# Kernel tuning notes

Hardware: AMD Instinct MI355X
Metric: run time of the kernel (lower is better)

The kernel has to match this reference:

```python
import jax, jax.numpy as jnp
import numpy as np

B = 65536
OBS_DIM = 85          # input_shape
FEAT = 8              # dim_entity_feature
NL = 5                # dim_landmarks
NT = 10               # dim_total
INF = 64              # in_features == out_features
HID = 64              # rnn_hidden_dim
NACT = 5              # n_actions
ALPHA = 0.01


def _leaky(x):
    return jnp.where(x > 0, x, ALPHA * x)


def setup_inputs() -> dict:
    key = jax.random.key(0)
    ks = jax.random.split(key, 26)
    s = 0.1
    d = {
        'obs': jax.random.normal(ks[0], (B, OBS_DIM), jnp.float32),
        'hidden_state': jax.random.normal(ks[1], (B, HID), jnp.float32),
        # entity input projections (input_layer_0/1/2), stored [in, out]
        'w_in0': jax.random.normal(ks[2], (FEAT, INF), jnp.float32) * s,
        'b_in0': jax.random.normal(ks[3], (INF,), jnp.float32) * s,
        'w_in1': jax.random.normal(ks[4], (FEAT, INF), jnp.float32) * s,
        'b_in1': jax.random.normal(ks[5], (INF,), jnp.float32) * s,
        'w_in2': jax.random.normal(ks[6], (FEAT, INF), jnp.float32) * s,
        'b_in2': jax.random.normal(ks[7], (INF,), jnp.float32) * s,
        # GAT params
        'W': jax.random.normal(ks[8], (INF, INF), jnp.float32) * s,
        'a': jax.random.normal(ks[9], (2 * INF, 1), jnp.float32) * s,
        # output MLP on attention rows (dim_soft = 2*dim_nearby = 10)
        'w_o1': jax.random.normal(ks[10], (2 * NL, 32), jnp.float32) * s,
        'b_o1': jax.random.normal(ks[11], (32,), jnp.float32) * s,
        'w_o2': jax.random.normal(ks[12], (32, 16), jnp.float32) * s,
        'b_o2': jax.random.normal(ks[13], (16,), jnp.float32) * s,
        'w_o3': jax.random.normal(ks[14], (16, 1), jnp.float32) * s,
        'b_o3': jax.random.normal(ks[15], (1,), jnp.float32) * s,
        # fc1 takes obs (85) concat atom_plug (5) -> 90
        'w_fc1': jax.random.normal(ks[16], (OBS_DIM + NL, HID), jnp.float32) * s,
        'b_fc1': jax.random.normal(ks[17], (HID,), jnp.float32) * s,
        # GRUCell, torch layout: [3H, in]
        'w_ih': jax.random.normal(ks[18], (3 * HID, HID), jnp.float32) * s,
        'w_hh': jax.random.normal(ks[19], (3 * HID, HID), jnp.float32) * s,
        'b_ih': jax.random.normal(ks[20], (3 * HID,), jnp.float32) * s,
        'b_hh': jax.random.normal(ks[21], (3 * HID,), jnp.float32) * s,
        'w_fc2': jax.random.normal(ks[22], (HID, NACT), jnp.float32) * s,
        'b_fc2': jax.random.normal(ks[23], (NACT,), jnp.float32) * s,
    }
    return d


def reference(obs, hidden_state, w_in0, b_in0, w_in1, b_in1, w_in2, b_in2,
              W, a, w_o1, b_o1, w_o2, b_o2, w_o3, b_o3,
              w_fc1, b_fc1, w_ih, w_hh, b_ih, b_hh, w_fc2, b_fc2):
    # data_preprocess: drop last dim_nearby cols, rotate first 4 to back, reshape to entities
    o = obs[:, :OBS_DIM - NL]                               # [B, 80]
    obs_in = jnp.concatenate([o[:, 4:], o[:, :4]], axis=-1).reshape(-1, NT, FEAT)  # [B,10,8]

    h0 = _leaky(obs_in @ w_in0 + b_in0)                     # [B,10,64]
    h1 = _leaky(obs_in @ w_in1 + b_in1)
    h2 = _leaky(obs_in @ w_in2 + b_in2)
    h_mix = jnp.concatenate([h0[:, :NL], h1[:, NL:NT - 1], h2[:, NT - 1:NT]], axis=1)  # [B,10,64]

    Wh = h_mix @ W                                          # [B,10,64]
    Wh1 = Wh @ a[:INF]                                      # [B,10,1]
    Wh2 = Wh @ a[INF:]                                      # [B,10,1]
    e = _leaky(Wh1 + jnp.swapaxes(Wh2, 1, 2))               # [B,10,10]

    att0 = jax.nn.softmax(e[:, :NL, NL:], axis=-1)          # [B,5,5]
    att1 = jnp.swapaxes(jax.nn.softmax(e[:, NL:, :NL], axis=-1), 1, 2)  # [B,5,5]
    attention = jnp.concatenate([att0, att1], axis=-1)      # [B,5,10]

    hp = _leaky(attention @ w_o1 + b_o1)
    hp = _leaky(hp @ w_o2 + b_o2)
    hp = _leaky(hp @ w_o3 + b_o3)[..., 0]                   # [B,5]
    obs_out = jax.nn.softmax(hp, axis=-1)                   # [B,5]

    obs_comb = jnp.concatenate([obs, obs_out], axis=-1)     # [B,90]
    x = jax.nn.relu(obs_comb @ w_fc1 + b_fc1)               # [B,64]

    h_in = hidden_state.reshape(-1, HID)
    gi = x @ w_ih.T + b_ih                                  # [B,192]
    gh = h_in @ w_hh.T + b_hh
    r = jax.nn.sigmoid(gi[:, :HID] + gh[:, :HID])
    z = jax.nn.sigmoid(gi[:, HID:2 * HID] + gh[:, HID:2 * HID])
    n = jnp.tanh(gi[:, 2 * HID:] + r * gh[:, 2 * HID:])
    h = (1.0 - z) * n + z * h_in                            # [B,64]

    q = h @ w_fc2 + b_fc2                                   # [B,5]
    return (q, h)
```

## Files before the change

### kernel.cpp

```cpp
#include <hip/hip_runtime.h>
#include <math.h>

namespace {

typedef __bf16 bf16x8 __attribute__((ext_vector_type(8)));
typedef __bf16 bf16x4 __attribute__((ext_vector_type(4)));
typedef float  f32x4  __attribute__((ext_vector_type(4)));
typedef float  f32x2  __attribute__((ext_vector_type(2)));

constexpr int B_      = 65536;
constexpr int OBS_DIM_= 85;
constexpr int NL_     = 5;
constexpr int NT_     = 10;
constexpr int HID_    = 64;
constexpr int NACT_   = 5;
constexpr float ALPHA_= 0.01f;

__device__ __forceinline__ float leaky(float x)    { return fmaf(fminf(x, 0.0f), ALPHA_ - 1.0f, x); }
__device__ __forceinline__ float sigmoidf(float x) { return 1.0f / (1.0f + __expf(-x)); }
__device__ __forceinline__ float tanh_fast(float x){ return 1.0f - 2.0f / (__expf(2.0f * x) + 1.0f); }

template <int CTRL>
__device__ __forceinline__ float dppadd(float x) {
  int y = __builtin_amdgcn_update_dpp(0, __float_as_int(x), CTRL, 0xF, 0xF, true);
  return x + __int_as_float(y);
}
__device__ __forceinline__ float red16(float x) {
  x = dppadd<0xB1>(x);
  x = dppadd<0x4E>(x);
  x = dppadd<0x141>(x);
  x = dppadd<0x140>(x);
  return x;
}

__global__ void prep_kernel(const float* __restrict__ W, const float* __restrict__ a,
                            const float* __restrict__ w_ih, const float* __restrict__ w_hh,
                            const float* __restrict__ w_fc1, void* __restrict__ ws) {
  float* Wa   = (float*)ws;
  __bf16* ih  = (__bf16*)((char*)ws + 512);
  __bf16* hh  = ih + 192 * 64;
  __bf16* f1t = hh + 192 * 64;
  const int tid = blockIdx.x * 256 + threadIdx.x;
  if (blockIdx.x == 0 && threadIdx.x < 64) {
    const int i = threadIdx.x;
    float s1 = 0.0f, s2 = 0.0f;
    #pragma unroll
    for (int j = 0; j < 64; ++j) {
      float w = W[i * 64 + j];
      s1 += w * a[j];
      s2 += w * a[64 + j];
    }
    Wa[i] = s1;
    Wa[64 + i] = s2;
  }
  const int stride = gridDim.x * 256;
  for (int i = tid; i < 192 * 64; i += stride) {
    int pr = i >> 6, k = i & 63;
    int g  = pr >> 6;
    int q  = pr & 63;
    int orig = (g << 6) + ((q & 15) << 2) + (q >> 4);
    ih[i] = (__bf16)w_ih[orig * 64 + k];
    hh[i] = (__bf16)w_hh[orig * 64 + k];
  }
  for (int i = tid; i < 64 * 96; i += stride) {
    int n = i / 96, k = i - 96 * n;
    float v = 0.0f;
    if (k < 85)                 v = w_fc1[k * 64 + n];
    else if (k >= 88 && k < 93) v = w_fc1[(85 + k - 88) * 64 + n];
    f1t[i] = (__bf16)v;
  }
}

constexpr int SXH_ = 72;

__global__ __launch_bounds__(256, 2) void fused_kernel(
    const float* __restrict__ obs, const float* __restrict__ hidden,
    const float* __restrict__ w_in0, const float* __restrict__ b_in0,
    const float* __restrict__ w_in1, const float* __restrict__ b_in1,
    const float* __restrict__ w_in2, const float* __restrict__ b_in2,
    const float* __restrict__ w_o1, const float* __restrict__ b_o1,
    const float* __restrict__ w_o2, const float* __restrict__ b_o2,
    const float* __restrict__ w_o3, const float* __restrict__ b_o3,
    const float* __restrict__ b_fc1,
    const float* __restrict__ b_ih, const float* __restrict__ b_hh,
    const float* __restrict__ w_fc2, const float* __restrict__ b_fc2,
    const void* __restrict__ wsv,
    float* __restrict__ q_out, float* __restrict__ h_out) {

  __shared__ __align__(16) char smem[28416];
  __bf16* s_obs          = (__bf16*)smem;
  float  (*s_att)[5][10] = (float (*)[5][10])(smem + 11264);
  __bf16 (*s_h1)[5][32]  = (__bf16 (*)[5][32])(smem + 14464);
  float  (*s_h2)[5][16]  = (float (*)[5][16])(smem + 19584);
  __bf16* A_x            = (__bf16*)(smem + 11264);
  float (*s_wh1)[12]     = (float (*)[12])(smem + 24704);
  float (*s_wh2)[12]     = (float (*)[12])(smem + 25472);
  float (*s_colm)[6]     = (float (*)[6])(smem + 26240);
  float (*s_cols)[6]     = (float (*)[6])(smem + 26624);
  float (*s_hp)[6]       = (float (*)[6])(smem + 27008);
  __bf16* s_o5           = (__bf16*)(smem + 27392);

  const int tid  = threadIdx.x;
  const int wv   = tid >> 6;
  const int lane = tid & 63;
  const int l16  = lane & 15;
  const int grp  = tid >> 4;
  const long gr0 = (long)blockIdx.x * 64;

  const float* Wa = (const float*)wsv;
  const __bf16* Wih = (const __bf16*)((const char*)wsv + 512);
  const __bf16* Whh = Wih + 192 * 64;
  const __bf16* Wf1 = Whh + 192 * 64;

  {
    const float* src = obs + gr0 * OBS_DIM_;
    const int base = wv * 340;
    #pragma unroll
    for (int k = 0; k < 6; ++k) {
      if (k < 5 || lane < 20) {
        int c = base + k * 64 + lane;
        f32x4 v = *(const f32x4*)&src[c * 4];
        #pragma unroll
        for (int e = 0; e < 4; ++e) {
          int fe = c * 4 + e;
          int r = fe / 85, col = fe - 85 * r;
          s_obs[r * 88 + col] = (__bf16)v[e];
        }
      }
    }
    if (lane < 48) {
      int r = wv * 16 + lane / 3, j = lane % 3;
      s_obs[r * 88 + 85 + j] = (__bf16)0.0f;
      s_o5[r * 8 + 5 + j]    = (__bf16)0.0f;
    }
  }

  const int u0 = l16 * 4;
  const f32x4 wa1 = *(const f32x4*)&Wa[u0];
  const f32x4 wa2 = *(const f32x4*)&Wa[64 + u0];

  __syncthreads();

  #pragma unroll 1
  for (int pass = 0; pass < 4; ++pass) {
    const int row = pass * 16 + grp;
    const __bf16* orow = s_obs + row * 88;

    f32x4 wA[8];
    f32x4 bA;
    #pragma unroll
    for (int t = 0; t < NT_; ++t) {
      if (t == 0) {
        #pragma unroll
        for (int f = 0; f < 8; ++f) wA[f] = *(const f32x4*)&w_in0[f * 64 + u0];
        bA = *(const f32x4*)&b_in0[u0];
      }
      if (t == 5) {
        #pragma unroll
        for (int f = 0; f < 8; ++f) wA[f] = *(const f32x4*)&w_in1[f * 64 + u0];
        bA = *(const f32x4*)&b_in1[u0];
      }
      if (t == 9) {
        #pragma unroll
        for (int f = 0; f < 8; ++f) wA[f] = *(const f32x4*)&w_in2[f * 64 + u0];
        bA = *(const f32x4*)&b_in2[u0];
      }
      const int ia = t * 8 + 4;
      int ib = t * 8 + 8;
      if (ib >= 80) ib = 0;
      bf16x4 va = *(const bf16x4*)&orow[ia];
      bf16x4 vb = *(const bf16x4*)&orow[ib];
      float oa[4], ob[4];
      #pragma unroll
      for (int e = 0; e < 4; ++e) { oa[e] = (float)va[e]; ob[e] = (float)vb[e]; }
      f32x4 z = bA;
      #pragma unroll
      for (int f = 0; f < 4; ++f) {
        z[0] += oa[f] * wA[f][0]; z[1] += oa[f] * wA[f][1];
        z[2] += oa[f] * wA[f][2]; z[3] += oa[f] * wA[f][3];
      }
      #pragma unroll
      for (int f = 4; f < 8; ++f) {
        z[0] += ob[f - 4] * wA[f][0]; z[1] += ob[f - 4] * wA[f][1];
        z[2] += ob[f - 4] * wA[f][2]; z[3] += ob[f - 4] * wA[f][3];
      }
      float h0 = leaky(z[0]), h1 = leaky(z[1]), h2 = leaky(z[2]), h3 = leaky(z[3]);
      float p1t = h0 * wa1[0] + h1 * wa1[1] + h2 * wa1[2] + h3 * wa1[3];
      float p2t = h0 * wa2[0] + h1 * wa2[1] + h2 * wa2[2] + h3 * wa2[3];
      p1t = red16(p1t);
      p2t = red16(p2t);
      if (l16 == 0) { s_wh1[grp][t] = p1t; s_wh2[grp][t] = p2t; }
    }

    if (l16 >= 5 && l16 < 10) {
      const int jj = l16 - 5;
      float w1v = s_wh1[grp][NL_ + jj];
      float ev[NL_], m = -1e30f;
      #pragma unroll
      for (int k = 0; k < NL_; ++k) { ev[k] = leaky(w1v + s_wh2[grp][k]); m = fmaxf(m, ev[k]); }
      float s = 0.0f;
      #pragma unroll
      for (int k = 0; k < NL_; ++k) s += __expf(ev[k] - m);
      s_colm[grp][jj] = m;
      s_cols[grp][jj] = s;
    }

    if (l16 < NL_) {
      const int r = l16;
      const float wh1_r = s_wh1[grp][r];
      const float wh2_r = s_wh2[grp][r];
      float ev[NL_], m = -1e30f;
      #pragma unroll
      for (int j = 0; j < NL_; ++j) { ev[j] = leaky(wh1_r + s_wh2[grp][NL_ + j]); m = fmaxf(m, ev[j]); }
      float a0[NL_], s = 0.0f;
      #pragma unroll
      for (int j = 0; j < NL_; ++j) { a0[j] = __expf(ev[j] - m); s += a0[j]; }
      float inv = 1.0f / s;
      #pragma unroll
      for (int j = 0; j < NL_; ++j) s_att[grp][r][j] = a0[j] * inv;
      #pragma unroll
      for (int jj = 0; jj < NL_; ++jj) {
        float e = leaky(s_wh1[grp][NL_ + jj] + wh2_r);
        s_att[grp][r][NL_ + jj] = __expf(e - s_colm[grp][jj]) / s_cols[grp][jj];
      }
    }

    {
      f32x2 w1c[NT_];
      #pragma unroll
      for (int k = 0; k < NT_; ++k) w1c[k] = *(const f32x2*)&w_o1[k * 32 + l16 * 2];
      const f32x2 b1 = *(const f32x2*)&b_o1[l16 * 2];
      #pragma unroll
      for (int r5 = 0; r5 < NL_; ++r5) {
        float za = b1[0], zb = b1[1];
        #pragma unroll
        for (int k2 = 0; k2 < 5; ++k2) {
          f32x2 at = *(const f32x2*)&s_att[grp][r5][k2 * 2];
          za += at[0] * w1c[2 * k2][0] + at[1] * w1c[2 * k2 + 1][0];
          zb += at[0] * w1c[2 * k2][1] + at[1] * w1c[2 * k2 + 1][1];
        }
        s_h1[grp][r5][l16 * 2]     = (__bf16)leaky(za);
        s_h1[grp][r5][l16 * 2 + 1] = (__bf16)leaky(zb);
      }
    }

    {
      float w2c[32];
      #pragma unroll
      for (int k = 0; k < 32; ++k) w2c[k] = w_o2[k * 16 + l16];
      const float b2 = b_o2[l16];
      #pragma unroll
      for (int r5 = 0; r5 < NL_; ++r5) {
        float z = b2;
        #pragma unroll
        for (int k4 = 0; k4 < 8; ++k4) {
          bf16x4 hv = *(const bf16x4*)&s_h1[grp][r5][k4 * 4];
          z += (float)hv[0] * w2c[4 * k4] + (float)hv[1] * w2c[4 * k4 + 1]
             + (float)hv[2] * w2c[4 * k4 + 2] + (float)hv[3] * w2c[4 * k4 + 3];
        }
        s_h2[grp][r5][l16] = leaky(z);
      }
    }

    if (l16 < NL_) {
      float z3 = b_o3[0];
      #pragma unroll
      for (int k4 = 0; k4 < 4; ++k4) {
        f32x4 hv = *(const f32x4*)&s_h2[grp][l16][k4 * 4];
        z3 += hv[0] * w_o3[4 * k4] + hv[1] * w_o3[4 * k4 + 1]
            + hv[2] * w_o3[4 * k4 + 2] + hv[3] * w_o3[4 * k4 + 3];
      }
      float hp_own = leaky(z3);
      s_hp[grp][l16] = hp_own;
      float m5 = -1e30f;
      #pragma unroll
      for (int j = 0; j < NL_; ++j) m5 = fmaxf(m5, s_hp[grp][j]);
      float ssum = 0.0f;
      #pragma unroll
      for (int j = 0; j < NL_; ++j) ssum += __expf(s_hp[grp][j] - m5);
      s_o5[row * 8 + l16] = (__bf16)(__expf(hp_own - m5) / ssum);
    }
  }

  __syncthreads();

  const int l    = l16;
  const int quad = lane >> 4;
  const int r0   = wv * 16;

  bf16x8 ah[2];
  {
    const float* hrow_g = hidden + (gr0 + r0 + l) * HID_;
    f32x4 vha0 = *(const f32x4*)&hrow_g[quad * 8];
    f32x4 vha1 = *(const f32x4*)&hrow_g[quad * 8 + 4];
    f32x4 vhb0 = *(const f32x4*)&hrow_g[32 + quad * 8];
    f32x4 vhb1 = *(const f32x4*)&hrow_g[32 + quad * 8 + 4];
    bf16x8 t;
    t[0] = (__bf16)vha0[0]; t[1] = (__bf16)vha0[1]; t[2] = (__bf16)vha0[2]; t[3] = (__bf16)vha0[3];
    t[4] = (__bf16)vha1[0]; t[5] = (__bf16)vha1[1]; t[6] = (__bf16)vha1[2]; t[7] = (__bf16)vha1[3];
    ah[0] = t;
    t[0] = (__bf16)vhb0[0]; t[1] = (__bf16)vhb0[1]; t[2] = (__bf16)vhb0[2]; t[3] = (__bf16)vhb0[3];
    t[4] = (__bf16)vhb1[0]; t[5] = (__bf16)vhb1[1]; t[6] = (__bf16)vhb1[2]; t[7] = (__bf16)vhb1[3];
    ah[1] = t;
  }

  const f32x4 zero4 = {0.0f, 0.0f, 0.0f, 0.0f};

  f32x4 cx[4];
  #pragma unroll
  for (int nt = 0; nt < 4; ++nt) cx[nt] = zero4;
  #pragma unroll
  for (int ks = 0; ks < 3; ++ks) {
    bf16x8 af;
    if (ks < 2)         af = *(const bf16x8*)&s_obs[(r0 + l) * 88 + ks * 32 + quad * 8];
    else if (quad < 3)  af = *(const bf16x8*)&s_obs[(r0 + l) * 88 + 64 + quad * 8];
    else                af = *(const bf16x8*)&s_o5[(r0 + l) * 8];
    #pragma unroll
    for (int nt = 0; nt < 4; ++nt) {
      bf16x8 bf = *(const bf16x8*)&Wf1[(nt * 16 + l) * 96 + ks * 32 + quad * 8];
      cx[nt] = __builtin_amdgcn_mfma_f32_16x16x32_bf16(af, bf, cx[nt], 0, 0, 0);
    }
  }
  #pragma unroll
  for (int nt = 0; nt < 4; ++nt) {
    float bias = b_fc1[nt * 16 + l];
    #pragma unroll
    for (int rg = 0; rg < 4; ++rg) {
      float xv = fmaxf(cx[nt][rg] + bias, 0.0f);
      A_x[(r0 + quad * 4 + rg) * SXH_ + nt * 16 + l] = (__bf16)xv;
    }
  }

  bf16x8 ax[2];
  #pragma unroll
  for (int ks = 0; ks < 2; ++ks)
    ax[ks] = *(const bf16x8*)&A_x[(r0 + l) * SXH_ + ks * 32 + quad * 8];

  f32x4 cr[4], ch[4];
  #pragma unroll
  for (int nt = 0; nt < 4; ++nt) { cr[nt] = zero4; ch[nt] = zero4; }
  #pragma unroll
  for (int nt = 0; nt < 4; ++nt) {
    #pragma unroll
    for (int ks = 0; ks < 2; ++ks) {
      bf16x8 bi = *(const bf16x8*)&Wih[(nt * 16 + l) * 64 + ks * 32 + quad * 8];
      cr[nt] = __builtin_amdgcn_mfma_f32_16x16x32_bf16(ax[ks], bi, cr[nt], 0, 0, 0);
      bf16x8 bh = *(const bf16x8*)&Whh[(nt * 16 + l) * 64 + ks * 32 + quad * 8];
      cr[nt] = __builtin_amdgcn_mfma_f32_16x16x32_bf16(ah[ks], bh, cr[nt], 0, 0, 0);
    }
    #pragma unroll
    for (int ks = 0; ks < 2; ++ks) {
      bf16x8 bh = *(const bf16x8*)&Whh[(128 + nt * 16 + l) * 64 + ks * 32 + quad * 8];
      ch[nt] = __builtin_amdgcn_mfma_f32_16x16x32_bf16(ah[ks], bh, ch[nt], 0, 0, 0);
    }
  }
  f32x4 rn[4];
  {
    f32x4 a0 = *(const f32x4*)&b_ih[4 * l];
    f32x4 a1 = *(const f32x4*)&b_hh[4 * l];
    f32x4 br4 = a0 + a1;
    f32x4 bhn4 = *(const f32x4*)&b_hh[128 + 4 * l];
    #pragma unroll
    for (int nt = 0; nt < 4; ++nt)
      #pragma unroll
      for (int rg = 0; rg < 4; ++rg) {
        float rr = sigmoidf(cr[nt][rg] + br4[nt]);
        rn[nt][rg] = rr * (ch[nt][rg] + bhn4[nt]);
      }
  }

  f32x4 cn[4];
  #pragma unroll
  for (int nt = 0; nt < 4; ++nt) cn[nt] = zero4;
  #pragma unroll
  for (int nt = 0; nt < 4; ++nt)
    #pragma unroll
    for (int ks = 0; ks < 2; ++ks) {
      bf16x8 bi = *(const bf16x8*)&Wih[(128 + nt * 16 + l) * 64 + ks * 32 + quad * 8];
      cn[nt] = __builtin_amdgcn_mfma_f32_16x16x32_bf16(ax[ks], bi, cn[nt], 0, 0, 0);
    }
  f32x4 nn[4];
  {
    f32x4 bin4 = *(const f32x4*)&b_ih[128 + 4 * l];
    #pragma unroll
    for (int nt = 0; nt < 4; ++nt)
      #pragma unroll
      for (int rg = 0; rg < 4; ++rg)
        nn[nt][rg] = tanh_fast(cn[nt][rg] + bin4[nt] + rn[nt][rg]);
  }

  f32x4 cz[4];
  #pragma unroll
  for (int nt = 0; nt < 4; ++nt) cz[nt] = zero4;
  #pragma unroll
  for (int nt = 0; nt < 4; ++nt)
    #pragma unroll
    for (int ks = 0; ks < 2; ++ks) {
      bf16x8 bi = *(const bf16x8*)&Wih[(64 + nt * 16 + l) * 64 + ks * 32 + quad * 8];
      cz[nt] = __builtin_amdgcn_mfma_f32_16x16x32_bf16(ax[ks], bi, cz[nt], 0, 0, 0);
      bf16x8 bh = *(const bf16x8*)&Whh[(64 + nt * 16 + l) * 64 + ks * 32 + quad * 8];
      cz[nt] = __builtin_amdgcn_mfma_f32_16x16x32_bf16(ah[ks], bh, cz[nt], 0, 0, 0);
    }

  const long grow = gr0 + r0 + quad * 4;
  f32x4 bz4;
  {
    f32x4 a0 = *(const f32x4*)&b_ih[64 + 4 * l];
    f32x4 a1 = *(const f32x4*)&b_hh[64 + 4 * l];
    bz4 = a0 + a1;
  }
  f32x4 w20[5];
  #pragma unroll
  for (int j = 0; j < 5; ++j) w20[j] = *(const f32x4*)&w_fc2[20 * l + 4 * j];

  #pragma unroll
  for (int rg = 0; rg < 4; ++rg) {
    f32x4 hold = *(const f32x4*)&hidden[(grow + rg) * HID_ + 4 * l];
    f32x4 hnew;
    float qp5[NACT_] = {0.0f, 0.0f, 0.0f, 0.0f, 0.0f};
    #pragma unroll
    for (int t = 0; t < 4; ++t) {
      float zz = sigmoidf(cz[t][rg] + bz4[t]);
      float hn = (1.0f - zz) * nn[t][rg] + zz * hold[t];
      hnew[t] = hn;
      #pragma unroll
      for (int c = 0; c < NACT_; ++c)
        qp5[c] += hn * w20[(5 * t + c) >> 2][(5 * t + c) & 3];
    }
    *(f32x4*)&h_out[(grow + rg) * HID_ + 4 * l] = hnew;
    #pragma unroll
    for (int c = 0; c < NACT_; ++c) qp5[c] = red16(qp5[c]);
    if (l < NACT_) {
      float qv = qp5[0];
      if (l == 1) qv = qp5[1];
      if (l == 2) qv = qp5[2];
      if (l == 3) qv = qp5[3];
      if (l == 4) qv = qp5[4];
      q_out[(grow + rg) * NACT_ + l] = qv + b_fc2[l];
    }
  }
}

}

extern "C" void kernel_launch(void* const* d_in, const int* in_sizes, int n_in,
                              void* d_out, int out_size, void* d_ws, size_t ws_size,
                              hipStream_t stream) {
  const float* obs    = (const float*)d_in[0];
  const float* hidden = (const float*)d_in[1];
  const float* w_in0  = (const float*)d_in[2];
  const float* b_in0  = (const float*)d_in[3];
  const float* w_in1  = (const float*)d_in[4];
  const float* b_in1  = (const float*)d_in[5];
  const float* w_in2  = (const float*)d_in[6];
  const float* b_in2  = (const float*)d_in[7];
  const float* W      = (const float*)d_in[8];
  const float* a      = (const float*)d_in[9];
  const float* w_o1   = (const float*)d_in[10];
  const float* b_o1   = (const float*)d_in[11];
  const float* w_o2   = (const float*)d_in[12];
  const float* b_o2   = (const float*)d_in[13];
  const float* w_o3   = (const float*)d_in[14];
  const float* b_o3   = (const float*)d_in[15];
  const float* w_fc1  = (const float*)d_in[16];
  const float* b_fc1  = (const float*)d_in[17];
  const float* w_ih   = (const float*)d_in[18];
  const float* w_hh   = (const float*)d_in[19];
  const float* b_ih   = (const float*)d_in[20];
  const float* b_hh   = (const float*)d_in[21];
  const float* w_fc2  = (const float*)d_in[22];
  const float* b_fc2  = (const float*)d_in[23];

  float* q_out = (float*)d_out;
  float* h_out = q_out + (long)B_ * NACT_;

  prep_kernel<<<48, 256, 0, stream>>>(W, a, w_ih, w_hh, w_fc1, d_ws);
  fused_kernel<<<B_ / 64, 256, 0, stream>>>(
      obs, hidden,
      w_in0, b_in0, w_in1, b_in1, w_in2, b_in2,
      w_o1, b_o1, w_o2, b_o2, w_o3, b_o3,
      b_fc1, b_ih, b_hh, w_fc2, b_fc2,
      d_ws, q_out, h_out);
}
```

Baseline: 190.3 us.

## Compute entity input projections with block-diagonal bf16 MFMA instead of scalar FMAs

Moves the per-entity 8->64 input projections out of a per-row scalar FMA loop and into MFMA 16x16x32 tiles, using block-diagonal packed weights built in the prep kernel. The obs buffer is rearranged in shared memory into a 96-wide row so that entity features line up with the MFMA K-chunks and the fc1 input, which removes the separate s_o5 buffer. The goal is to cut VALU work and repeated global weight loads in the attention front-end. In exchange it performs redundant multiplies on zero blocks, holds more accumulator registers, and uses more shared memory.

```diff
diff --git a/kernel.cpp b/kernel.cpp
--- a/kernel.cpp
+++ b/kernel.cpp
@@ -35,11 +35,14 @@
 
 __global__ void prep_kernel(const float* __restrict__ W, const float* __restrict__ a,
                             const float* __restrict__ w_ih, const float* __restrict__ w_hh,
-                            const float* __restrict__ w_fc1, void* __restrict__ ws) {
+                            const float* __restrict__ w_fc1,
+                            const float* __restrict__ w_in0, const float* __restrict__ w_in1,
+                            const float* __restrict__ w_in2, void* __restrict__ ws) {
   float* Wa   = (float*)ws;
   __bf16* ih  = (__bf16*)((char*)ws + 512);
   __bf16* hh  = ih + 192 * 64;
   __bf16* f1t = hh + 192 * 64;
+  __bf16* wst = f1t + 64 * 96;
   const int tid = blockIdx.x * 256 + threadIdx.x;
   if (blockIdx.x == 0 && threadIdx.x < 64) {
     const int i = threadIdx.x;
@@ -65,19 +68,36 @@
   for (int i = tid; i < 64 * 96; i += stride) {
     int n = i / 96, k = i - 96 * n;
     float v = 0.0f;
-    if (k < 85)                 v = w_fc1[k * 64 + n];
+    if (k < 76)                 v = w_fc1[(4 + k) * 64 + n];
+    else if (k < 80)            v = w_fc1[(k - 76) * 64 + n];
+    else if (k < 85)            v = w_fc1[k * 64 + n];
     else if (k >= 88 && k < 93) v = w_fc1[(85 + k - 88) * 64 + n];
     f1t[i] = (__bf16)v;
   }
+  for (int i = tid; i < 20480; i += stride) {
+    int g, c;
+    if (i < 8192)       { g = 0; c = i >> 5; }
+    else if (i < 16384) { g = 1; c = (i - 8192) >> 5; }
+    else                { g = 2; c = (i - 16384) >> 5; }
+    int k = i & 31;
+    int t_loc = c >> 6, u = c & 63;
+    int t_k = k >> 3, f = k & 7;
+    float v = 0.0f;
+    if (t_k == t_loc) {
+      int t = g * 4 + t_loc;
+      const float* w = (t < 5) ? w_in0 : (t < 9 ? w_in1 : w_in2);
+      v = w[f * 64 + u];
+    }
+    wst[i] = (__bf16)v;
+  }
 }
 
 constexpr int SXH_ = 72;
 
 __global__ __launch_bounds__(256, 2) void fused_kernel(
     const float* __restrict__ obs, const float* __restrict__ hidden,
-    const float* __restrict__ w_in0, const float* __restrict__ b_in0,
-    const float* __restrict__ w_in1, const float* __restrict__ b_in1,
-    const float* __restrict__ w_in2, const float* __restrict__ b_in2,
+    const float* __restrict__ b_in0, const float* __restrict__ b_in1,
+    const float* __restrict__ b_in2,
     const float* __restrict__ w_o1, const float* __restrict__ b_o1,
     const float* __restrict__ w_o2, const float* __restrict__ b_o2,
     const float* __restrict__ w_o3, const float* __restrict__ b_o3,
@@ -87,30 +107,32 @@
     const void* __restrict__ wsv,
     float* __restrict__ q_out, float* __restrict__ h_out) {
 
-  __shared__ __align__(16) char smem[28416];
-  __bf16* s_obs          = (__bf16*)smem;
-  float  (*s_att)[5][10] = (float (*)[5][10])(smem + 11264);
-  __bf16 (*s_h1)[5][32]  = (__bf16 (*)[5][32])(smem + 14464);
-  float  (*s_h2)[5][16]  = (float (*)[5][16])(smem + 19584);
-  __bf16* A_x            = (__bf16*)(smem + 11264);
-  float (*s_wh1)[12]     = (float (*)[12])(smem + 24704);
-  float (*s_wh2)[12]     = (float (*)[12])(smem + 25472);
-  float (*s_colm)[6]     = (float (*)[6])(smem + 26240);
-  float (*s_cols)[6]     = (float (*)[6])(smem + 26624);
-  float (*s_hp)[6]       = (float (*)[6])(smem + 27008);
-  __bf16* s_o5           = (__bf16*)(smem + 27392);
+  __shared__ __align__(16) char smem[33024];
+  __bf16* s_oin          = (__bf16*)smem;
+  float (*s_wh1)[12]     = (float (*)[12])(smem + 12288);
+  float (*s_wh2)[12]     = (float (*)[12])(smem + 15360);
+  float  (*s_att)[5][10] = (float (*)[5][10])(smem + 18432);
+  __bf16 (*s_h1)[5][32]  = (__bf16 (*)[5][32])(smem + 21632);
+  float  (*s_h2)[5][16]  = (float (*)[5][16])(smem + 26752);
+  float (*s_colm)[6]     = (float (*)[6])(smem + 31872);
+  float (*s_cols)[6]     = (float (*)[6])(smem + 32256);
+  float (*s_hp)[6]       = (float (*)[6])(smem + 32640);
+  __bf16* A_x            = (__bf16*)(smem + 18432);
 
   const int tid  = threadIdx.x;
   const int wv   = tid >> 6;
   const int lane = tid & 63;
   const int l16  = lane & 15;
+  const int quad = lane >> 4;
   const int grp  = tid >> 4;
+  const int r0   = wv * 16;
   const long gr0 = (long)blockIdx.x * 64;
 
   const float* Wa = (const float*)wsv;
   const __bf16* Wih = (const __bf16*)((const char*)wsv + 512);
   const __bf16* Whh = Wih + 192 * 64;
   const __bf16* Wf1 = Whh + 192 * 64;
+  const __bf16* Wst = Wf1 + 64 * 96;
 
   {
     const float* src = obs + gr0 * OBS_DIM_;
@@ -118,86 +140,83 @@
     #pragma unroll
     for (int k = 0; k < 6; ++k) {
       if (k < 5 || lane < 20) {
-        int c = base + k * 64 + lane;
-        f32x4 v = *(const f32x4*)&src[c * 4];
+        int c4 = base + k * 64 + lane;
+        f32x4 v = *(const f32x4*)&src[c4 * 4];
         #pragma unroll
         for (int e = 0; e < 4; ++e) {
-          int fe = c * 4 + e;
-          int r = fe / 85, col = fe - 85 * r;
-          s_obs[r * 88 + col] = (__bf16)v[e];
+          int fe = c4 * 4 + e;
+          int r = fe / 85, c = fe - 85 * r;
+          int j = (c < 4) ? (76 + c) : ((c >= 80) ? c : (c - 4));
+          s_oin[r * 96 + j] = (__bf16)v[e];
         }
       }
     }
-    if (lane < 48) {
-      int r = wv * 16 + lane / 3, j = lane % 3;
-      s_obs[r * 88 + 85 + j] = (__bf16)0.0f;
-      s_o5[r * 8 + 5 + j]    = (__bf16)0.0f;
-    }
-  }
-
-  const int u0 = l16 * 4;
-  const f32x4 wa1 = *(const f32x4*)&Wa[u0];
-  const f32x4 wa2 = *(const f32x4*)&Wa[64 + u0];
+    for (int i2 = tid; i2 < 704; i2 += 256) {
+      int r = i2 / 11, j = 85 + i2 % 11;
+      s_oin[r * 96 + j] = (__bf16)0.0f;
+    }
+  }
+
+  __syncthreads();
+
+  {
+    float wa1v[4], wa2v[4], bcl[3][4];
+    #pragma unroll
+    for (int nt = 0; nt < 4; ++nt) {
+      wa1v[nt] = Wa[nt * 16 + l16];
+      wa2v[nt] = Wa[64 + nt * 16 + l16];
+      bcl[0][nt] = b_in0[nt * 16 + l16];
+      bcl[1][nt] = b_in1[nt * 16 + l16];
+      bcl[2][nt] = b_in2[nt * 16 + l16];
+    }
+    const f32x4 zero4 = {0.0f, 0.0f, 0.0f, 0.0f};
+    #pragma unroll
+    for (int g = 0; g < 3; ++g) {
+      const int NCT = (g == 2) ? 8 : 16;
+      bf16x8 af = *(const bf16x8*)&s_oin[(r0 + l16) * 96 + g * 32 + quad * 8];
+      f32x4 cst[16];
+      #pragma unroll
+      for (int ct = 0; ct < NCT; ++ct) {
+        bf16x8 bf = *(const bf16x8*)&Wst[g * 8192 + (ct * 16 + l16) * 32 + quad * 8];
+        cst[ct] = __builtin_amdgcn_mfma_f32_16x16x32_bf16(af, bf, zero4, 0, 0, 0);
+      }
+      const int NTL = (g == 2) ? 2 : 4;
+      #pragma unroll
+      for (int t_loc = 0; t_loc < NTL; ++t_loc) {
+        const int t = g * 4 + t_loc;
+        const int cls = (t < 5) ? 0 : ((t < 9) ? 1 : 2);
+        #pragma unroll
+        for (int rg = 0; rg < 4; ++rg) {
+          float p1 = 0.0f, p2 = 0.0f;
+          #pragma unroll
+          for (int nt = 0; nt < 4; ++nt) {
+            float v = leaky(cst[t_loc * 4 + nt][rg] + bcl[cls][nt]);
+            p1 = fmaf(v, wa1v[nt], p1);
+            p2 = fmaf(v, wa2v[nt], p2);
+          }
+          p1 = red16(p1);
+          p2 = red16(p2);
+          if (l16 == 0) {
+            s_wh1[r0 + quad * 4 + rg][t] = p1;
+            s_wh2[r0 + quad * 4 + rg][t] = p2;
+          }
+        }
+      }
+    }
+  }
 
   __syncthreads();
 
   #pragma unroll 1
   for (int pass = 0; pass < 4; ++pass) {
     const int row = pass * 16 + grp;
-    const __bf16* orow = s_obs + row * 88;
-
-    f32x4 wA[8];
-    f32x4 bA;
-    #pragma unroll
-    for (int t = 0; t < NT_; ++t) {
-      if (t == 0) {
-        #pragma unroll
-        for (int f = 0; f < 8; ++f) wA[f] = *(const f32x4*)&w_in0[f * 64 + u0];
-        bA = *(const f32x4*)&b_in0[u0];
-      }
-      if (t == 5) {
-        #pragma unroll
-        for (int f = 0; f < 8; ++f) wA[f] = *(const f32x4*)&w_in1[f * 64 + u0];
-        bA = *(const f32x4*)&b_in1[u0];
-      }
-      if (t == 9) {
-        #pragma unroll
-        for (int f = 0; f < 8; ++f) wA[f] = *(const f32x4*)&w_in2[f * 64 + u0];
-        bA = *(const f32x4*)&b_in2[u0];
-      }
-      const int ia = t * 8 + 4;
-      int ib = t * 8 + 8;
-      if (ib >= 80) ib = 0;
-      bf16x4 va = *(const bf16x4*)&orow[ia];
-      bf16x4 vb = *(const bf16x4*)&orow[ib];
-      float oa[4], ob[4];
-      #pragma unroll
-      for (int e = 0; e < 4; ++e) { oa[e] = (float)va[e]; ob[e] = (float)vb[e]; }
-      f32x4 z = bA;
-      #pragma unroll
-      for (int f = 0; f < 4; ++f) {
-        z[0] += oa[f] * wA[f][0]; z[1] += oa[f] * wA[f][1];
-        z[2] += oa[f] * wA[f][2]; z[3] += oa[f] * wA[f][3];
-      }
-      #pragma unroll
-      for (int f = 4; f < 8; ++f) {
-        z[0] += ob[f - 4] * wA[f][0]; z[1] += ob[f - 4] * wA[f][1];
-        z[2] += ob[f - 4] * wA[f][2]; z[3] += ob[f - 4] * wA[f][3];
-      }
-      float h0 = leaky(z[0]), h1 = leaky(z[1]), h2 = leaky(z[2]), h3 = leaky(z[3]);
-      float p1t = h0 * wa1[0] + h1 * wa1[1] + h2 * wa1[2] + h3 * wa1[3];
-      float p2t = h0 * wa2[0] + h1 * wa2[1] + h2 * wa2[2] + h3 * wa2[3];
-      p1t = red16(p1t);
-      p2t = red16(p2t);
-      if (l16 == 0) { s_wh1[grp][t] = p1t; s_wh2[grp][t] = p2t; }
-    }
 
     if (l16 >= 5 && l16 < 10) {
       const int jj = l16 - 5;
-      float w1v = s_wh1[grp][NL_ + jj];
+      float w1v = s_wh1[row][NL_ + jj];
       float ev[NL_], m = -1e30f;
       #pragma unroll
-      for (int k = 0; k < NL_; ++k) { ev[k] = leaky(w1v + s_wh2[grp][k]); m = fmaxf(m, ev[k]); }
+      for (int k = 0; k < NL_; ++k) { ev[k] = leaky(w1v + s_wh2[row][k]); m = fmaxf(m, ev[k]); }
       float s = 0.0f;
       #pragma unroll
       for (int k = 0; k < NL_; ++k) s += __expf(ev[k] - m);
@@ -207,11 +226,11 @@
 
     if (l16 < NL_) {
       const int r = l16;
-      const float wh1_r = s_wh1[grp][r];
-      const float wh2_r = s_wh2[grp][r];
+      const float wh1_r = s_wh1[row][r];
+      const float wh2_r = s_wh2[row][r];
       float ev[NL_], m = -1e30f;
       #pragma unroll
-      for (int j = 0; j < NL_; ++j) { ev[j] = leaky(wh1_r + s_wh2[grp][NL_ + j]); m = fmaxf(m, ev[j]); }
+      for (int j = 0; j < NL_; ++j) { ev[j] = leaky(wh1_r + s_wh2[row][NL_ + j]); m = fmaxf(m, ev[j]); }
       float a0[NL_], s = 0.0f;
       #pragma unroll
       for (int j = 0; j < NL_; ++j) { a0[j] = __expf(ev[j] - m); s += a0[j]; }
@@ -220,7 +239,7 @@
       for (int j = 0; j < NL_; ++j) s_att[grp][r][j] = a0[j] * inv;
       #pragma unroll
       for (int jj = 0; jj < NL_; ++jj) {
-        float e = leaky(s_wh1[grp][NL_ + jj] + wh2_r);
+        float e = leaky(s_wh1[row][NL_ + jj] + wh2_r);
         s_att[grp][r][NL_ + jj] = __expf(e - s_colm[grp][jj]) / s_cols[grp][jj];
       }
     }
@@ -278,15 +297,13 @@
       float ssum = 0.0f;
       #pragma unroll
       for (int j = 0; j < NL_; ++j) ssum += __expf(s_hp[grp][j] - m5);
-      s_o5[row * 8 + l16] = (__bf16)(__expf(hp_own - m5) / ssum);
+      s_oin[row * 96 + 88 + l16] = (__bf16)(__expf(hp_own - m5) / ssum);
     }
   }
 
   __syncthreads();
 
-  const int l    = l16;
-  const int quad = lane >> 4;
-  const int r0   = wv * 16;
+  const int l = l16;
 
   bf16x8 ah[2];
   {
@@ -311,10 +328,7 @@
   for (int nt = 0; nt < 4; ++nt) cx[nt] = zero4;
   #pragma unroll
   for (int ks = 0; ks < 3; ++ks) {
-    bf16x8 af;
-    if (ks < 2)         af = *(const bf16x8*)&s_obs[(r0 + l) * 88 + ks * 32 + quad * 8];
-    else if (quad < 3)  af = *(const bf16x8*)&s_obs[(r0 + l) * 88 + 64 + quad * 8];
-    else                af = *(const bf16x8*)&s_o5[(r0 + l) * 8];
+    bf16x8 af = *(const bf16x8*)&s_oin[(r0 + l) * 96 + ks * 32 + quad * 8];
     #pragma unroll
     for (int nt = 0; nt < 4; ++nt) {
       bf16x8 bf = *(const bf16x8*)&Wf1[(nt * 16 + l) * 96 + ks * 32 + quad * 8];
@@ -474,10 +488,10 @@
   float* q_out = (float*)d_out;
   float* h_out = q_out + (long)B_ * NACT_;
 
-  prep_kernel<<<48, 256, 0, stream>>>(W, a, w_ih, w_hh, w_fc1, d_ws);
+  prep_kernel<<<48, 256, 0, stream>>>(W, a, w_ih, w_hh, w_fc1, w_in0, w_in1, w_in2, d_ws);
   fused_kernel<<<B_ / 64, 256, 0, stream>>>(
       obs, hidden,
-      w_in0, b_in0, w_in1, b_in1, w_in2, b_in2,
+      b_in0, b_in1, b_in2,
       w_o1, b_o1, w_o2, b_o2, w_o3, b_o3,
       b_fc1, b_ih, b_hh, w_fc2, b_fc2,
       d_ws, q_out, h_out);
```

Result: slower. 221.7 us (+16.5%).
